# Optimization experiments

Measured on AMD Instinct MI355X. Metric: run time of the kernel, lower is better.

## Reference

```python
import jax, jax.numpy as jnp
import numpy as np
import math

H = 16  # number of heads (init kwarg h)
EPS = 1e-6


def _apply_kernel(x, orf):
    # x: [B, h, L, d_k], orf: [m, d_k]
    m, d_k = orf.shape
    proj = jnp.einsum('bhld,md->bhlm', x, orf) / (d_k ** 0.25)
    norm = jnp.sum(x * x, axis=-1, keepdims=True) / (2.0 * math.sqrt(d_k))
    return (jnp.exp(proj - norm) + EPS) / math.sqrt(m)


def setup_inputs() -> dict:
    key = jax.random.key(0)
    ks = jax.random.split(key, 10)
    B, L, D, m = 4, 4096, 1024, 256
    d_k = D // H
    s = 1.0 / math.sqrt(D)
    return {
        'x': jax.random.normal(ks[0], (B, L, D), jnp.float32),
        'Wq': jax.random.normal(ks[1], (D, D), jnp.float32) * s,
        'bq': jax.random.normal(ks[2], (D,), jnp.float32) * s,
        'Wk': jax.random.normal(ks[3], (D, D), jnp.float32) * s,
        'bk': jax.random.normal(ks[4], (D,), jnp.float32) * s,
        'Wv': jax.random.normal(ks[5], (D, D), jnp.float32) * s,
        'bv': jax.random.normal(ks[6], (D,), jnp.float32) * s,
        'Wo': jax.random.normal(ks[7], (D, D), jnp.float32) * s,
        'bo': jax.random.normal(ks[8], (D,), jnp.float32) * s,
        'orf': jax.random.normal(ks[9], (m, d_k), jnp.float32),
    }


def reference(x, Wq, bq, Wk, bk, Wv, bv, Wo, bo, orf):
    B, L, D = x.shape
    d_k = D // H

    def split(y):  # [B, L, D] -> [B, h, L, d_k]
        return y.reshape(B, L, H, d_k).transpose(0, 2, 1, 3)

    q = split(x @ Wq.T + bq)
    k = split(x @ Wk.T + bk)
    v = split(x @ Wv.T + bv)

    q_phi = _apply_kernel(q, orf)  # [B, h, L, m]
    k_phi = _apply_kernel(k, orf)  # [B, h, L, m]

    # FAVOR+ linear attention: O(L*m*d_k)
    kv = jnp.einsum('bhlm,bhld->bhmd', k_phi, v)      # [B, h, m, d_k]
    ksum = jnp.sum(k_phi, axis=2)                      # [B, h, m]
    num = jnp.einsum('bhlm,bhmd->bhld', q_phi, kv)     # [B, h, L, d_k]
    den = jnp.einsum('bhlm,bhm->bhl', q_phi, ksum)     # [B, h, L]
    out = num / den[..., None]

    out = out.transpose(0, 2, 1, 3).reshape(B, L, D)   # concat heads
    return out @ Wo.T + bo
```

## Files before the change

### kernel.cpp

```cpp
#include <hip/hip_runtime.h>
#include <math.h>

#define HH 16
#define BB 4
#define LL 4096
#define DD 1024
#define DK 64
#define MMF 256
#define EPSF 1e-6f
#define KSCALE (0.35355339059327373f * 1.4426950408889634f)
#define NORMSCALE (0.0625f * 1.4426950408889634f)
#define NSPLIT 8
#define LCH (LL / NSPLIT)

typedef __attribute__((ext_vector_type(8))) short bf16x8;
typedef __attribute__((ext_vector_type(4))) float f32x4;
typedef __attribute__((ext_vector_type(8))) unsigned short u16x8;

__device__ __forceinline__ unsigned short f2bf(float f) {
  union { float f; unsigned u; } v; v.f = f;
  unsigned r = v.u + 0x7FFF + ((v.u >> 16) & 1);
  return (unsigned short)(r >> 16);
}
__device__ __forceinline__ float bf2f(unsigned short h) {
  union { unsigned u; float f; } v; v.u = ((unsigned)h) << 16;
  return v.f;
}
__device__ __forceinline__ f32x4 mfma16(bf16x8 a, bf16x8 b, f32x4 c) {
  return __builtin_amdgcn_mfma_f32_16x16x32_bf16(a, b, c, 0, 0, 0);
}
__device__ __forceinline__ float fexp2(float x) {
  return __builtin_amdgcn_exp2f(x);
}
__device__ __forceinline__ void gload16(const unsigned short* g, unsigned short* l) {
  __builtin_amdgcn_global_load_lds(
      (const __attribute__((address_space(1))) void*)g,
      (__attribute__((address_space(3))) void*)l, 16, 0, 0);
}
#define SWZ(row, col) ((col) ^ (((row) & 7) << 3))

__global__ __launch_bounds__(256) void cvt_bf16(
    const float* __restrict__ src, unsigned short* __restrict__ dst, int n) {
  int i = (blockIdx.x * 256 + threadIdx.x) * 4;
  if (i < n) {
    float4 v = *(const float4*)&src[i];
    ushort4 o;
    o.x = f2bf(v.x); o.y = f2bf(v.y); o.z = f2bf(v.z); o.w = f2bf(v.w);
    *(ushort4*)&dst[i] = o;
  }
}

__global__ __launch_bounds__(256) void cvt_bf16_w(
    const float* __restrict__ W0, const float* __restrict__ W1,
    const float* __restrict__ W2, const float* __restrict__ W3,
    unsigned short* __restrict__ D0, unsigned short* __restrict__ D1,
    unsigned short* __restrict__ D2, unsigned short* __restrict__ D3) {
  const float* s;
  unsigned short* d;
  switch (blockIdx.y) {
    case 0: s = W0; d = D0; break;
    case 1: s = W1; d = D1; break;
    case 2: s = W2; d = D2; break;
    default: s = W3; d = D3; break;
  }
  int i = (blockIdx.x * 256 + threadIdx.x) * 4;
  float4 v = *(const float4*)&s[i];
  ushort4 o;
  o.x = f2bf(v.x); o.y = f2bf(v.y); o.z = f2bf(v.z); o.w = f2bf(v.w);
  *(ushort4*)&d[i] = o;
}

__global__ __launch_bounds__(256) void cvt_orf(
    const float* __restrict__ src, unsigned short* __restrict__ hi, int n) {
  int i = blockIdx.x * 256 + threadIdx.x;
  if (i < n) hi[i] = f2bf(src[i] * KSCALE);
}

template <int MODE>
__global__ __launch_bounds__(256) void gemm_mfma(
    const unsigned short* __restrict__ A, const unsigned short* __restrict__ W,
    const float* __restrict__ bias, float* __restrict__ Cf,
    unsigned short* __restrict__ C1, unsigned short* __restrict__ C2,
    float* __restrict__ Cn, int M, int N, int K) {
  __shared__ __align__(16) char smem[65536];
  unsigned short* S = (unsigned short*)smem;
  const int tid = threadIdx.x, lane = tid & 63;
  const int w = tid >> 6, wr = w >> 1, wc = w & 1;
  const int g = lane >> 4, li = lane & 15;
  const int flat = blockIdx.y * gridDim.x + blockIdx.x;
  const int xcd = flat & 7, loc = flat >> 3;
  const int m0 = ((xcd << 4) + (loc & 15)) * 128;
  const int n0 = (loc >> 4) * 128;

  f32x4 acc[4][4] = {};
  const int srow8 = lane >> 3;
  const int scol  = ((lane & 7) ^ srow8) << 3;
  const unsigned short* Ag = A + (size_t)(m0 + w * 32 + srow8) * K + scol;
  const unsigned short* Wg = W + (size_t)(n0 + w * 32 + srow8) * K + scol;
  const int nt = K >> 6;

#pragma unroll
  for (int j = 0; j < 4; ++j) {
    gload16(Ag + (size_t)j * 8 * K, S + (w * 32 + j * 8) * 64);
    gload16(Wg + (size_t)j * 8 * K, S + 8192 + (w * 32 + j * 8) * 64);
  }

  for (int t = 0; t < nt; ++t) {
    const int co = (t & 1) << 14;
    const int no = co ^ 16384;
    if (t + 1 < nt) {
      const int k1 = (t + 1) << 6;
#pragma unroll
      for (int j = 0; j < 4; ++j) {
        gload16(Ag + (size_t)j * 8 * K + k1, S + no + (w * 32 + j * 8) * 64);
        gload16(Wg + (size_t)j * 8 * K + k1, S + no + 8192 + (w * 32 + j * 8) * 64);
      }
      asm volatile("s_waitcnt vmcnt(8)" ::: "memory");
    } else {
      asm volatile("s_waitcnt vmcnt(0)" ::: "memory");
    }
    __builtin_amdgcn_s_barrier();

    const int sx = (li & 7) << 3;
#pragma unroll
    for (int kk = 0; kk < 2; ++kk) {
      const int c = (kk * 32 + g * 8) ^ sx;
      bf16x8 af[4], bfr[4];
#pragma unroll
      for (int i = 0; i < 4; ++i)
        af[i] = *(const bf16x8*)&S[co + (wr * 64 + i * 16 + li) * 64 + c];
#pragma unroll
      for (int j = 0; j < 4; ++j)
        bfr[j] = *(const bf16x8*)&S[co + 8192 + (wc * 64 + j * 16 + li) * 64 + c];
#pragma unroll
      for (int i = 0; i < 4; ++i)
#pragma unroll
        for (int j = 0; j < 4; ++j)
          acc[i][j] = mfma16(af[i], bfr[j], acc[i][j]);
    }
    asm volatile("s_waitcnt lgkmcnt(0)" ::: "memory");
    __builtin_amdgcn_s_barrier();
  }

  float* ep = (float*)smem + w * (32 * 68);
  const int head = (n0 + wc * 64) >> 6;
  const int rbase = m0 + wr * 64;
  const int b = rbase >> 12;

  if (MODE == 2) {
#pragma unroll
    for (int jh = 0; jh < 2; ++jh) {
#pragma unroll
      for (int i2 = 0; i2 < 2; ++i2) {
        const int i = jh * 2 + i2;
#pragma unroll
        for (int j = 0; j < 4; ++j) {
          const float bz = bias[n0 + wc * 64 + j * 16 + li];
#pragma unroll
          for (int r = 0; r < 4; ++r)
            ep[(i2 * 16 + 4 * g + r) * 68 + j * 16 + li] = acc[i][j][r] + bz;
        }
      }
      const int rrow = lane >> 3, cc = lane & 7;
#pragma unroll
      for (int p = 0; p < 4; ++p) {
        const int row = p * 8 + rrow;
        float v[8];
        *(f32x4*)&v[0] = *(const f32x4*)&ep[row * 68 + cc * 8];
        *(f32x4*)&v[4] = *(const f32x4*)&ep[row * 68 + cc * 8 + 4];
        float np = 0.f;
        u16x8 hv, lv;
#pragma unroll
        for (int e = 0; e < 8; ++e) {
          float vv = v[e];
          np += vv * vv;
          unsigned short h = f2bf(vv);
          hv[e] = h;
          lv[e] = f2bf(vv - bf2f(h));
        }
        const int lg = (rbase + jh * 32 + row) & 4095;
        const size_t rowb = (size_t)(b * 16 + head) * 4096 + lg;
        *(u16x8*)&C1[rowb * 64 + cc * 8] = hv;
        *(u16x8*)&C2[rowb * 64 + cc * 8] = lv;
        np += __shfl_xor(np, 1);
        np += __shfl_xor(np, 2);
        np += __shfl_xor(np, 4);
        if (cc == 0) Cn[rowb] = np * NORMSCALE;
      }
    }
  } else if (MODE == 1) {
#pragma unroll
    for (int jh = 0; jh < 2; ++jh) {
#pragma unroll
      for (int i = 0; i < 4; ++i)
#pragma unroll
        for (int j2 = 0; j2 < 2; ++j2) {
          const int j = jh * 2 + j2;
          const float bz = bias[n0 + wc * 64 + j * 16 + li];
          f32x4 t;
          t[0] = acc[i][j][0] + bz; t[1] = acc[i][j][1] + bz;
          t[2] = acc[i][j][2] + bz; t[3] = acc[i][j][3] + bz;
          *(f32x4*)&ep[(j2 * 16 + li) * 68 + i * 16 + 4 * g] = t;
        }
      const int rd = lane >> 3, cc = lane & 7;
#pragma unroll
      for (int p = 0; p < 4; ++p) {
        const int dl = p * 8 + rd;
        float v[8];
        *(f32x4*)&v[0] = *(const f32x4*)&ep[dl * 68 + cc * 8];
        *(f32x4*)&v[4] = *(const f32x4*)&ep[dl * 68 + cc * 8 + 4];
        u16x8 hv;
#pragma unroll
        for (int e = 0; e < 8; ++e) hv[e] = f2bf(v[e]);
        const int dh = jh * 32 + dl;
        const int lg = rbase & 4095;
        *(u16x8*)&C1[((size_t)(b * 16 + head) * 64 + dh) * 4096 + lg + cc * 8] = hv;
      }
    }
  } else {
#pragma unroll
    for (int jh = 0; jh < 2; ++jh) {
#pragma unroll
      for (int i2 = 0; i2 < 2; ++i2) {
        const int i = jh * 2 + i2;
#pragma unroll
        for (int j = 0; j < 4; ++j) {
          const float bz = bias[n0 + wc * 64 + j * 16 + li];
#pragma unroll
          for (int r = 0; r < 4; ++r)
            ep[(i2 * 16 + 4 * g + r) * 68 + j * 16 + li] = acc[i][j][r] + bz;
        }
      }
      const int rrow = lane >> 4, cc = lane & 15;
#pragma unroll
      for (int p = 0; p < 8; ++p) {
        const int row = p * 4 + rrow;
        f32x4 v = *(const f32x4*)&ep[row * 68 + cc * 4];
        *(f32x4*)&Cf[(size_t)(rbase + jh * 32 + row) * 1024 + n0 + wc * 64 + cc * 4] = v;
      }
    }
  }
}

__global__ __launch_bounds__(256, 2) void kv_mfma(
    const unsigned short* __restrict__ khi, const unsigned short* __restrict__ klo,
    const float* __restrict__ knorms, const unsigned short* __restrict__ vt,
    const unsigned short* __restrict__ orfhi,
    float* __restrict__ pkv, float* __restrict__ pksum) {
  __shared__ __align__(16) unsigned short KsHi[64 * 64], KsLo[64 * 64];
  __shared__ __align__(16) unsigned short VT[64 * 64], KphiT[64 * 64];
  __shared__ float ns[64];
  const int tid = threadIdx.x, lane = tid & 63, w = tid >> 6;
  const int g = lane >> 4, li = lane & 15;
  const int bh = blockIdx.x, sp = blockIdx.y;
  const int srow8 = lane >> 3;
  const int scol  = ((lane & 7) ^ srow8) << 3;
  const int sx = (li & 7) << 3;

  bf16x8 oh[4][2];
#pragma unroll
  for (int p = 0; p < 4; ++p)
#pragma unroll
    for (int kk = 0; kk < 2; ++kk)
      oh[p][kk] = *(const bf16x8*)
          &orfhi[(size_t)(p * 64 + w * 16 + li) * 64 + kk * 32 + g * 8];

  f32x4 kvacc[4][4] = {};
  float ksacc[4][4] = {};

  for (int c = 0; c < LCH / 64; ++c) {
    const int l0 = sp * LCH + c * 64;
    __syncthreads();
    {
      const size_t kb = ((size_t)bh * 4096 + l0 + w * 16 + srow8) * 64 + scol;
      gload16(khi + kb, &KsHi[(w * 16) * 64]);
      gload16(khi + kb + 8 * 64, &KsHi[(w * 16 + 8) * 64]);
      gload16(klo + kb, &KsLo[(w * 16) * 64]);
      gload16(klo + kb + 8 * 64, &KsLo[(w * 16 + 8) * 64]);
      const size_t vb = ((size_t)bh * 64 + w * 16 + srow8) * 4096 + l0 + scol;
      gload16(vt + vb, &VT[(w * 16) * 64]);
      gload16(vt + vb + (size_t)8 * 4096, &VT[(w * 16 + 8) * 64]);
      if (tid < 64) ns[tid] = knorms[(size_t)bh * 4096 + l0 + tid];
    }
    __syncthreads();

#pragma unroll
    for (int p = 0; p < 4; ++p) {
      f32x4 pr[4] = {};
      __builtin_amdgcn_s_setprio(1);
#pragma unroll
      for (int kk = 0; kk < 2; ++kk) {
        const int cx = (kk * 32 + g * 8) ^ sx;
#pragma unroll
        for (int lf = 0; lf < 4; ++lf) {
          const bf16x8 bh2 = *(const bf16x8*)&KsHi[(lf * 16 + li) * 64 + cx];
          const bf16x8 bl2 = *(const bf16x8*)&KsLo[(lf * 16 + li) * 64 + cx];
          pr[lf] = mfma16(oh[p][kk], bh2, pr[lf]);
          pr[lf] = mfma16(oh[p][kk], bl2, pr[lf]);
        }
      }
      __builtin_amdgcn_s_setprio(0);
#pragma unroll
      for (int lf = 0; lf < 4; ++lf) {
        const float nrm = ns[lf * 16 + li];
#pragma unroll
        for (int r = 0; r < 4; ++r) {
          float phi = fexp2(pr[lf][r] - nrm) + EPSF;
          ksacc[p][r] += phi;
          const int row = w * 16 + 4 * g + r;
          KphiT[row * 64 + SWZ(row, lf * 16 + li)] = f2bf(phi);
        }
      }
      __builtin_amdgcn_s_setprio(1);
#pragma unroll
      for (int kk = 0; kk < 2; ++kk) {
        const int cx = (kk * 32 + g * 8) ^ sx;
        const bf16x8 a = *(const bf16x8*)&KphiT[(w * 16 + li) * 64 + cx];
#pragma unroll
        for (int df = 0; df < 4; ++df) {
          const bf16x8 bv = *(const bf16x8*)&VT[(df * 16 + li) * 64 + cx];
          kvacc[p][df] = mfma16(a, bv, kvacc[p][df]);
        }
      }
      __builtin_amdgcn_s_setprio(0);
    }
  }
  float* kvo = pkv + ((size_t)sp * 64 + bh) * (MMF * DK);
#pragma unroll
  for (int p = 0; p < 4; ++p)
#pragma unroll
    for (int df = 0; df < 4; ++df)
#pragma unroll
      for (int r = 0; r < 4; ++r)
        kvo[(p * 64 + w * 16 + 4 * g + r) * DK + df * 16 + li] = kvacc[p][df][r];

  float* kso = pksum + ((size_t)sp * 64 + bh) * MMF;
#pragma unroll
  for (int p = 0; p < 4; ++p)
#pragma unroll
    for (int r = 0; r < 4; ++r) {
      float s = ksacc[p][r];
      s += __shfl_xor(s, 1); s += __shfl_xor(s, 2);
      s += __shfl_xor(s, 4); s += __shfl_xor(s, 8);
      if (li == 0) kso[p * 64 + w * 16 + 4 * g + r] = s;
    }
}

__global__ __launch_bounds__(256) void reduce_parts(
    const float* __restrict__ pkv, unsigned short* __restrict__ kvT,
    const float* __restrict__ pks, float* __restrict__ ksg) {
  const int id = blockIdx.x * 256 + threadIdx.x;
  {
    const int bh = id >> 12, rest = id & 4095;
    const int m0 = (rest >> 6) << 2, d = rest & 63;
    float s0 = 0.f, s1 = 0.f, s2 = 0.f, s3 = 0.f;
#pragma unroll
    for (int sp = 0; sp < NSPLIT; ++sp) {
      const float* p = pkv + (size_t)(sp * 64 + bh) * (MMF * DK) + d;
      s0 += p[(m0 + 0) * DK]; s1 += p[(m0 + 1) * DK];
      s2 += p[(m0 + 2) * DK]; s3 += p[(m0 + 3) * DK];
    }
    ushort4 o;
    o.x = f2bf(s0); o.y = f2bf(s1); o.z = f2bf(s2); o.w = f2bf(s3);
    *(ushort4*)&kvT[((size_t)bh * DK + d) * MMF + m0] = o;
  }
  if (id < 4096) {
    float4 s = {0.f, 0.f, 0.f, 0.f};
#pragma unroll
    for (int sp = 0; sp < NSPLIT; ++sp) {
      float4 v = *(const float4*)&pks[(size_t)sp * 64 * MMF + id * 4];
      s.x += v.x; s.y += v.y; s.z += v.z; s.w += v.w;
    }
    *(float4*)&ksg[id * 4] = s;
  }
}

__global__ __launch_bounds__(512, 4) void qattn_mfma(
    const unsigned short* __restrict__ qhi, const unsigned short* __restrict__ qlo,
    const float* __restrict__ qnorms,
    const unsigned short* __restrict__ orfhi,
    const unsigned short* __restrict__ kvT, const float* __restrict__ ksg,
    unsigned short* __restrict__ attn) {
  __shared__ __align__(16) unsigned short OHi[256 * 64];
  __shared__ __align__(16) unsigned short KvTs[64 * 256];
  __shared__ __align__(16) unsigned short Qphi[8][16 * 64];
  const int tid = threadIdx.x, lane = tid & 63, w = tid >> 6;
  const int g = lane >> 4, li = lane & 15;
  const int bh = blockIdx.x, lb = blockIdx.y;
  const int b = bh >> 4, h = bh & 15;
  const int srow8 = lane >> 3;
  const int scol  = ((lane & 7) ^ srow8) << 3;
  const int sx = (li & 7) << 3;

#pragma unroll
  for (int q = 0; q < 4; ++q) {
    const size_t o = (size_t)(w * 32 + q * 8 + srow8) * 64 + scol;
    gload16(orfhi + o, &OHi[(w * 32 + q * 8) * 64]);
  }
  {
    const int srow2 = lane >> 5;
#pragma unroll
    for (int q = 0; q < 4; ++q) {
      const int d0 = w * 8 + q * 2, dr = d0 + srow2;
      gload16(kvT + ((size_t)bh * DK + dr) * MMF + (((lane & 31) ^ (dr & 7)) << 3),
              &KvTs[d0 * 256]);
    }
  }

  float ksr[4][4];
#pragma unroll
  for (int p = 0; p < 4; ++p)
#pragma unroll
    for (int mf = 0; mf < 4; ++mf)
      ksr[p][mf] = ksg[(size_t)bh * MMF + p * 64 + mf * 16 + li];
  const float4 nr =
      *(const float4*)&qnorms[(size_t)bh * 4096 + lb * 128 + w * 16 + 4 * g];
  bf16x8 qh[2], ql[2];
  {
    const size_t qr = ((size_t)bh * 4096 + lb * 128 + w * 16 + li) * 64 + g * 8;
    qh[0] = *(const bf16x8*)&qhi[qr];
    qh[1] = *(const bf16x8*)&qhi[qr + 32];
    ql[0] = *(const bf16x8*)&qlo[qr];
    ql[1] = *(const bf16x8*)&qlo[qr + 32];
  }
  __syncthreads();

  f32x4 numacc[4] = {};
  float denacc[4] = {};

#pragma unroll
  for (int p = 0; p < 4; ++p) {
    f32x4 pr[4] = {};
    __builtin_amdgcn_s_setprio(1);
#pragma unroll
    for (int kk = 0; kk < 2; ++kk) {
      const int cx = (kk * 32 + g * 8) ^ sx;
#pragma unroll
      for (int mf = 0; mf < 4; ++mf) {
        const int row = p * 64 + mf * 16 + li;
        const bf16x8 bh2 = *(const bf16x8*)&OHi[row * 64 + cx];
        pr[mf] = mfma16(qh[kk], bh2, pr[mf]);
        pr[mf] = mfma16(ql[kk], bh2, pr[mf]);
      }
    }
    __builtin_amdgcn_s_setprio(0);
#pragma unroll
    for (int mf = 0; mf < 4; ++mf) {
      const float ks = ksr[p][mf];
#pragma unroll
      for (int r = 0; r < 4; ++r) {
        float phi = fexp2(pr[mf][r] - nr[r]) + EPSF;
        denacc[r] += phi * ks;
        const int row = 4 * g + r;
        Qphi[w][row * 64 + SWZ(row, mf * 16 + li)] = f2bf(phi);
      }
    }
    __builtin_amdgcn_s_setprio(1);
#pragma unroll
    for (int kk = 0; kk < 2; ++kk) {
      const int cx = (kk * 32 + g * 8) ^ sx;
      const bf16x8 a = *(const bf16x8*)&Qphi[w][li * 64 + cx];
#pragma unroll
      for (int df = 0; df < 4; ++df) {
        const bf16x8 bv = *(const bf16x8*)
            &KvTs[(df * 16 + li) * 256 + (((p * 8 + kk * 4 + g) ^ (li & 7)) << 3)];
        numacc[df] = mfma16(a, bv, numacc[df]);
      }
    }
    __builtin_amdgcn_s_setprio(0);
  }
  float den[4];
#pragma unroll
  for (int r = 0; r < 4; ++r) {
    float s = denacc[r];
    s += __shfl_xor(s, 1); s += __shfl_xor(s, 2);
    s += __shfl_xor(s, 4); s += __shfl_xor(s, 8);
    den[r] = s;
  }
  unsigned short* ab =
      attn + ((size_t)b * 4096 + lb * 128) * 1024 + h * 64;
#pragma unroll
  for (int df = 0; df < 4; ++df)
#pragma unroll
    for (int r = 0; r < 4; ++r)
      ab[(size_t)(w * 16 + 4 * g + r) * 1024 + df * 16 + li] =
          f2bf(numacc[df][r] / den[r]);
}

extern "C" void kernel_launch(void* const* d_in, const int* in_sizes, int n_in,
                              void* d_out, int out_size, void* d_ws, size_t ws_size,
                              hipStream_t stream) {
  (void)in_sizes; (void)n_in; (void)out_size; (void)ws_size;
  const float* x   = (const float*)d_in[0];
  const float* Wq  = (const float*)d_in[1];
  const float* bq  = (const float*)d_in[2];
  const float* Wk  = (const float*)d_in[3];
  const float* bk  = (const float*)d_in[4];
  const float* Wv  = (const float*)d_in[5];
  const float* bv  = (const float*)d_in[6];
  const float* Wo  = (const float*)d_in[7];
  const float* bo  = (const float*)d_in[8];
  const float* orf = (const float*)d_in[9];
  float* out = (float*)d_out;

  const size_t ND = (size_t)BB * LL * DD;
  char* base = (char*)d_ws;
  size_t off = 0;
  auto alloc = [&](size_t bytes) -> char* {
    char* p = base + off;
    off += (bytes + 255) & ~(size_t)255;
    return p;
  };
  unsigned short* wqbf   = (unsigned short*)alloc((size_t)DD * DD * 2);
  unsigned short* wkbf   = (unsigned short*)alloc((size_t)DD * DD * 2);
  unsigned short* wvbf   = (unsigned short*)alloc((size_t)DD * DD * 2);
  unsigned short* wobf   = (unsigned short*)alloc((size_t)DD * DD * 2);
  unsigned short* orfhi  = (unsigned short*)alloc((size_t)MMF * DK * 2);
  unsigned short* xbf    = (unsigned short*)alloc(ND * 2);
  unsigned short* qhi    = (unsigned short*)alloc(ND * 2);
  unsigned short* qlo    = (unsigned short*)alloc(ND * 2);
  unsigned short* khi    = (unsigned short*)alloc(ND * 2);
  unsigned short* klo    = (unsigned short*)alloc(ND * 2);
  unsigned short* vtbuf  = (unsigned short*)alloc(ND * 2);
  float*          qnorms = (float*)alloc((size_t)64 * LL * 4);
  float*          knorms = (float*)alloc((size_t)64 * LL * 4);
  float*          pksum  = (float*)alloc((size_t)NSPLIT * 64 * MMF * 4);
  unsigned short* kvT    = (unsigned short*)alloc((size_t)64 * DK * MMF * 2);
  float*          ksg    = (float*)alloc((size_t)64 * MMF * 4);
  float*          pkv    = (float*)xbf;
  unsigned short* attnbf = khi;

  cvt_bf16<<<16384, 256, 0, stream>>>(x, xbf, (int)ND);
  cvt_bf16_w<<<dim3(1024, 4), 256, 0, stream>>>(Wq, Wk, Wv, Wo,
                                                wqbf, wkbf, wvbf, wobf);
  cvt_orf<<<64, 256, 0, stream>>>(orf, orfhi, MMF * DK);

  dim3 gg(128, 8);
  gemm_mfma<2><<<gg, 256, 0, stream>>>(xbf, wqbf, bq, (float*)0, qhi, qlo,
                                       qnorms, BB * LL, DD, DD);
  gemm_mfma<2><<<gg, 256, 0, stream>>>(xbf, wkbf, bk, (float*)0, khi, klo,
                                       knorms, BB * LL, DD, DD);
  gemm_mfma<1><<<gg, 256, 0, stream>>>(xbf, wvbf, bv, (float*)0, vtbuf,
                                       (unsigned short*)0, (float*)0,
                                       BB * LL, DD, DD);

  kv_mfma<<<dim3(64, NSPLIT), 256, 0, stream>>>(khi, klo, knorms, vtbuf,
                                                orfhi, pkv, pksum);
  reduce_parts<<<1024, 256, 0, stream>>>(pkv, kvT, pksum, ksg);
  qattn_mfma<<<dim3(64, 32), 512, 0, stream>>>(qhi, qlo, qnorms, orfhi,
                                               kvT, ksg, attnbf);

  gemm_mfma<0><<<gg, 256, 0, stream>>>(attnbf, wobf, bo, out, (unsigned short*)0,
                                       (unsigned short*)0, (float*)0,
                                       BB * LL, DD, DD);
}
```

Before: 298.4 us.

## Enlarge GEMM tiles to 256x256 with 8-wave blocks and restructured pipeline

Each of the four projection GEMMs now uses a 256x256 output tile with 512 threads (8 waves, each computing 128x64), a 128KB LDS double buffer, and split k-halves separated by barriers. MFMA sections are wrapped in s_setprio and the epilogues are adjusted for the larger tile, adding barriers between reuses of the LDS staging area. The aim is to raise arithmetic intensity and cut global/LDS traffic per FLOP. In exchange it uses more registers and LDS per block, leaving at most one block per CU and only 256 blocks for 256 CUs, which may cost occupancy and latency hiding.

Measured after the change: 286.5 us. -4.0%, faster.

```diff
diff --git a/kernel.cpp b/kernel.cpp
--- a/kernel.cpp
+++ b/kernel.cpp
@@ -77,85 +77,103 @@
 }
 
 template <int MODE>
-__global__ __launch_bounds__(256) void gemm_mfma(
+__global__ __launch_bounds__(512, 2) void gemm_mfma(
     const unsigned short* __restrict__ A, const unsigned short* __restrict__ W,
     const float* __restrict__ bias, float* __restrict__ Cf,
     unsigned short* __restrict__ C1, unsigned short* __restrict__ C2,
     float* __restrict__ Cn, int M, int N, int K) {
-  __shared__ __align__(16) char smem[65536];
+  __shared__ __align__(16) char smem[131072];
   unsigned short* S = (unsigned short*)smem;
   const int tid = threadIdx.x, lane = tid & 63;
-  const int w = tid >> 6, wr = w >> 1, wc = w & 1;
+  const int w = tid >> 6;
+  const int wm = w >> 2, wn = w & 3;
   const int g = lane >> 4, li = lane & 15;
   const int flat = blockIdx.y * gridDim.x + blockIdx.x;
   const int xcd = flat & 7, loc = flat >> 3;
-  const int m0 = ((xcd << 4) + (loc & 15)) * 128;
-  const int n0 = (loc >> 4) * 128;
-
-  f32x4 acc[4][4] = {};
+  const int m0 = (xcd * 8 + (loc & 7)) * 256;
+  const int n0 = (loc >> 3) * 256;
+
+  f32x4 acc[8][4] = {};
   const int srow8 = lane >> 3;
   const int scol  = ((lane & 7) ^ srow8) << 3;
-  const unsigned short* Ag = A + (size_t)(m0 + w * 32 + srow8) * K + scol;
-  const unsigned short* Wg = W + (size_t)(n0 + w * 32 + srow8) * K + scol;
+  const unsigned short* Ast = A + (size_t)(m0 + w * 32 + srow8) * K + scol;
+  const unsigned short* Wst = W + (size_t)(n0 + w * 32 + srow8) * K + scol;
   const int nt = K >> 6;
-
-#pragma unroll
-  for (int j = 0; j < 4; ++j) {
-    gload16(Ag + (size_t)j * 8 * K, S + (w * 32 + j * 8) * 64);
-    gload16(Wg + (size_t)j * 8 * K, S + 8192 + (w * 32 + j * 8) * 64);
-  }
-
-  for (int t = 0; t < nt; ++t) {
-    const int co = (t & 1) << 14;
-    const int no = co ^ 16384;
-    if (t + 1 < nt) {
-      const int k1 = (t + 1) << 6;
-#pragma unroll
-      for (int j = 0; j < 4; ++j) {
-        gload16(Ag + (size_t)j * 8 * K + k1, S + no + (w * 32 + j * 8) * 64);
-        gload16(Wg + (size_t)j * 8 * K + k1, S + no + 8192 + (w * 32 + j * 8) * 64);
-      }
-      asm volatile("s_waitcnt vmcnt(8)" ::: "memory");
-    } else {
-      asm volatile("s_waitcnt vmcnt(0)" ::: "memory");
-    }
-    __builtin_amdgcn_s_barrier();
-
-    const int sx = (li & 7) << 3;
-#pragma unroll
-    for (int kk = 0; kk < 2; ++kk) {
-      const int c = (kk * 32 + g * 8) ^ sx;
-      bf16x8 af[4], bfr[4];
-#pragma unroll
-      for (int i = 0; i < 4; ++i)
-        af[i] = *(const bf16x8*)&S[co + (wr * 64 + i * 16 + li) * 64 + c];
+  const int sx = (li & 7) << 3;
+
+#pragma unroll
+  for (int gi = 0; gi < 4; ++gi) {
+    gload16(Ast + (size_t)gi * 8 * K, S + (w * 32 + gi * 8) * 64);
+    gload16(Wst + (size_t)gi * 8 * K, S + 16384 + (w * 32 + gi * 8) * 64);
+  }
+  asm volatile("s_waitcnt vmcnt(0)" ::: "memory");
+  __builtin_amdgcn_s_barrier();
+
+  for (int kt = 0; kt < nt; ++kt) {
+    const int co = (kt & 1) << 15;
+    const int no = co ^ 32768;
+    if (kt + 1 < nt) {
+      const size_t k1 = (size_t)(kt + 1) << 6;
+#pragma unroll
+      for (int gi = 0; gi < 4; ++gi) {
+        gload16(Ast + (size_t)gi * 8 * K + k1, S + no + (w * 32 + gi * 8) * 64);
+        gload16(Wst + (size_t)gi * 8 * K + k1,
+                S + no + 16384 + (w * 32 + gi * 8) * 64);
+      }
+    }
+    {
+      const int c = (g * 8) ^ sx;
+      bf16x8 af[8], bfr[4];
+#pragma unroll
+      for (int i = 0; i < 8; ++i)
+        af[i] = *(const bf16x8*)&S[co + (wm * 128 + i * 16 + li) * 64 + c];
 #pragma unroll
       for (int j = 0; j < 4; ++j)
-        bfr[j] = *(const bf16x8*)&S[co + 8192 + (wc * 64 + j * 16 + li) * 64 + c];
-#pragma unroll
-      for (int i = 0; i < 4; ++i)
+        bfr[j] = *(const bf16x8*)&S[co + 16384 + (wn * 64 + j * 16 + li) * 64 + c];
+      __builtin_amdgcn_s_setprio(1);
+#pragma unroll
+      for (int i = 0; i < 8; ++i)
 #pragma unroll
         for (int j = 0; j < 4; ++j)
           acc[i][j] = mfma16(af[i], bfr[j], acc[i][j]);
-    }
-    asm volatile("s_waitcnt lgkmcnt(0)" ::: "memory");
+      __builtin_amdgcn_s_setprio(0);
+    }
     __builtin_amdgcn_s_barrier();
+    {
+      const int c = (32 + g * 8) ^ sx;
+      bf16x8 af[8], bfr[4];
+#pragma unroll
+      for (int i = 0; i < 8; ++i)
+        af[i] = *(const bf16x8*)&S[co + (wm * 128 + i * 16 + li) * 64 + c];
+#pragma unroll
+      for (int j = 0; j < 4; ++j)
+        bfr[j] = *(const bf16x8*)&S[co + 16384 + (wn * 64 + j * 16 + li) * 64 + c];
+      __builtin_amdgcn_s_setprio(1);
+#pragma unroll
+      for (int i = 0; i < 8; ++i)
+#pragma unroll
+        for (int j = 0; j < 4; ++j)
+          acc[i][j] = mfma16(af[i], bfr[j], acc[i][j]);
+      __builtin_amdgcn_s_setprio(0);
+    }
+    if (kt + 1 < nt) asm volatile("s_waitcnt vmcnt(0)" ::: "memory");
+    __builtin_amdgcn_s_barrier();
   }
 
   float* ep = (float*)smem + w * (32 * 68);
-  const int head = (n0 + wc * 64) >> 6;
-  const int rbase = m0 + wr * 64;
+  const int head = (n0 + wn * 64) >> 6;
+  const int rbase = m0 + wm * 128;
   const int b = rbase >> 12;
 
   if (MODE == 2) {
 #pragma unroll
-    for (int jh = 0; jh < 2; ++jh) {
+    for (int jh = 0; jh < 4; ++jh) {
 #pragma unroll
       for (int i2 = 0; i2 < 2; ++i2) {
         const int i = jh * 2 + i2;
 #pragma unroll
         for (int j = 0; j < 4; ++j) {
-          const float bz = bias[n0 + wc * 64 + j * 16 + li];
+          const float bz = bias[n0 + wn * 64 + j * 16 + li];
 #pragma unroll
           for (int r = 0; r < 4; ++r)
             ep[(i2 * 16 + 4 * g + r) * 68 + j * 16 + li] = acc[i][j][r] + bz;
@@ -187,45 +205,52 @@
         np += __shfl_xor(np, 4);
         if (cc == 0) Cn[rowb] = np * NORMSCALE;
       }
+      __builtin_amdgcn_s_barrier();
     }
   } else if (MODE == 1) {
 #pragma unroll
     for (int jh = 0; jh < 2; ++jh) {
 #pragma unroll
-      for (int i = 0; i < 4; ++i)
-#pragma unroll
-        for (int j2 = 0; j2 < 2; ++j2) {
-          const int j = jh * 2 + j2;
-          const float bz = bias[n0 + wc * 64 + j * 16 + li];
-          f32x4 t;
-          t[0] = acc[i][j][0] + bz; t[1] = acc[i][j][1] + bz;
-          t[2] = acc[i][j][2] + bz; t[3] = acc[i][j][3] + bz;
-          *(f32x4*)&ep[(j2 * 16 + li) * 68 + i * 16 + 4 * g] = t;
-        }
-      const int rd = lane >> 3, cc = lane & 7;
-#pragma unroll
-      for (int p = 0; p < 4; ++p) {
-        const int dl = p * 8 + rd;
-        float v[8];
-        *(f32x4*)&v[0] = *(const f32x4*)&ep[dl * 68 + cc * 8];
-        *(f32x4*)&v[4] = *(const f32x4*)&ep[dl * 68 + cc * 8 + 4];
-        u16x8 hv;
-#pragma unroll
-        for (int e = 0; e < 8; ++e) hv[e] = f2bf(v[e]);
-        const int dh = jh * 32 + dl;
-        const int lg = rbase & 4095;
-        *(u16x8*)&C1[((size_t)(b * 16 + head) * 64 + dh) * 4096 + lg + cc * 8] = hv;
+      for (int lh = 0; lh < 2; ++lh) {
+#pragma unroll
+        for (int i2 = 0; i2 < 4; ++i2) {
+          const int i = lh * 4 + i2;
+#pragma unroll
+          for (int j2 = 0; j2 < 2; ++j2) {
+            const int j = jh * 2 + j2;
+            const float bz = bias[n0 + wn * 64 + j * 16 + li];
+            f32x4 t;
+            t[0] = acc[i][j][0] + bz; t[1] = acc[i][j][1] + bz;
+            t[2] = acc[i][j][2] + bz; t[3] = acc[i][j][3] + bz;
+            *(f32x4*)&ep[(j2 * 16 + li) * 68 + i2 * 16 + 4 * g] = t;
+          }
+        }
+        const int rd = lane >> 3, cc = lane & 7;
+#pragma unroll
+        for (int p = 0; p < 4; ++p) {
+          const int dl = p * 8 + rd;
+          float v[8];
+          *(f32x4*)&v[0] = *(const f32x4*)&ep[dl * 68 + cc * 8];
+          *(f32x4*)&v[4] = *(const f32x4*)&ep[dl * 68 + cc * 8 + 4];
+          u16x8 hv;
+#pragma unroll
+          for (int e = 0; e < 8; ++e) hv[e] = f2bf(v[e]);
+          const int dh = jh * 32 + dl;
+          const int lg = (rbase + lh * 64) & 4095;
+          *(u16x8*)&C1[((size_t)(b * 16 + head) * 64 + dh) * 4096 + lg + cc * 8] = hv;
+        }
+        __builtin_amdgcn_s_barrier();
       }
     }
   } else {
 #pragma unroll
-    for (int jh = 0; jh < 2; ++jh) {
+    for (int jh = 0; jh < 4; ++jh) {
 #pragma unroll
       for (int i2 = 0; i2 < 2; ++i2) {
         const int i = jh * 2 + i2;
 #pragma unroll
         for (int j = 0; j < 4; ++j) {
-          const float bz = bias[n0 + wc * 64 + j * 16 + li];
+          const float bz = bias[n0 + wn * 64 + j * 16 + li];
 #pragma unroll
           for (int r = 0; r < 4; ++r)
             ep[(i2 * 16 + 4 * g + r) * 68 + j * 16 + li] = acc[i][j][r] + bz;
@@ -236,8 +261,9 @@
       for (int p = 0; p < 8; ++p) {
         const int row = p * 4 + rrow;
         f32x4 v = *(const f32x4*)&ep[row * 68 + cc * 4];
-        *(f32x4*)&Cf[(size_t)(rbase + jh * 32 + row) * 1024 + n0 + wc * 64 + cc * 4] = v;
-      }
+        *(f32x4*)&Cf[(size_t)(rbase + jh * 32 + row) * 1024 + n0 + wn * 64 + cc * 4] = v;
+      }
+      __builtin_amdgcn_s_barrier();
     }
   }
 }
@@ -535,12 +561,12 @@
                                                 wqbf, wkbf, wvbf, wobf);
   cvt_orf<<<64, 256, 0, stream>>>(orf, orfhi, MMF * DK);
 
-  dim3 gg(128, 8);
-  gemm_mfma<2><<<gg, 256, 0, stream>>>(xbf, wqbf, bq, (float*)0, qhi, qlo,
+  dim3 gg(64, 4);
+  gemm_mfma<2><<<gg, 512, 0, stream>>>(xbf, wqbf, bq, (float*)0, qhi, qlo,
                                        qnorms, BB * LL, DD, DD);
-  gemm_mfma<2><<<gg, 256, 0, stream>>>(xbf, wkbf, bk, (float*)0, khi, klo,
+  gemm_mfma<2><<<gg, 512, 0, stream>>>(xbf, wkbf, bk, (float*)0, khi, klo,
                                        knorms, BB * LL, DD, DD);
-  gemm_mfma<1><<<gg, 256, 0, stream>>>(xbf, wvbf, bv, (float*)0, vtbuf,
+  gemm_mfma<1><<<gg, 512, 0, stream>>>(xbf, wvbf, bv, (float*)0, vtbuf,
                                        (unsigned short*)0, (float*)0,
                                        BB * LL, DD, DD);
 
@@ -550,7 +576,7 @@
   qattn_mfma<<<dim3(64, 32), 512, 0, stream>>>(qhi, qlo, qnorms, orfhi,
                                                kvT, ksg, attnbf);
 
-  gemm_mfma<0><<<gg, 256, 0, stream>>>(attnbf, wobf, bo, out, (unsigned short*)0,
+  gemm_mfma<0><<<gg, 512, 0, stream>>>(attnbf, wobf, bo, out, (unsigned short*)0,
                                        (unsigned short*)0, (float*)0,
                                        BB * LL, DD, DD);
 }
```

## Use 256x128 GEMM tiles with 512 threads and a triple-buffered LDS pipeline

Applied to the files above, without the earlier changes.

Reworks the bf16 MFMA GEMM used for the Q/K/V/O projections. Each block now computes a 256x128 output tile with 8 waves instead of 128x128 with 4 waves, which halves the grid and cuts the W traffic per output. The double-buffered K loop becomes a three-stage LDS pipeline that prefetches two tiles ahead. The MFMA sections are wrapped in s_setprio. The cost is 144KB of LDS per block, which likely limits each CU to one block and lowers occupancy.

Measured after the change: 303.9 us. Within noise of the previous version (+1.8%).

```diff
diff --git a/kernel.cpp b/kernel.cpp
--- a/kernel.cpp
+++ b/kernel.cpp
@@ -77,74 +77,82 @@
 }
 
 template <int MODE>
-__global__ __launch_bounds__(256) void gemm_mfma(
+__global__ __launch_bounds__(512, 2) void gemm_mfma(
     const unsigned short* __restrict__ A, const unsigned short* __restrict__ W,
     const float* __restrict__ bias, float* __restrict__ Cf,
     unsigned short* __restrict__ C1, unsigned short* __restrict__ C2,
     float* __restrict__ Cn, int M, int N, int K) {
-  __shared__ __align__(16) char smem[65536];
+  __shared__ __align__(16) char smem[147456];
   unsigned short* S = (unsigned short*)smem;
   const int tid = threadIdx.x, lane = tid & 63;
-  const int w = tid >> 6, wr = w >> 1, wc = w & 1;
+  const int w = tid >> 6;
+  const int wm = w >> 1, wn = w & 1;
   const int g = lane >> 4, li = lane & 15;
   const int flat = blockIdx.y * gridDim.x + blockIdx.x;
   const int xcd = flat & 7, loc = flat >> 3;
-  const int m0 = ((xcd << 4) + (loc & 15)) * 128;
-  const int n0 = (loc >> 4) * 128;
+  const int m0 = (xcd * 8 + (loc & 7)) * 256;
+  const int n0 = (loc >> 3) * 128;
 
   f32x4 acc[4][4] = {};
   const int srow8 = lane >> 3;
   const int scol  = ((lane & 7) ^ srow8) << 3;
-  const unsigned short* Ag = A + (size_t)(m0 + w * 32 + srow8) * K + scol;
-  const unsigned short* Wg = W + (size_t)(n0 + w * 32 + srow8) * K + scol;
+  const unsigned short* Ast = A + (size_t)(m0 + w * 32 + srow8) * K + scol;
+  const unsigned short* Wst = W + (size_t)(n0 + w * 16 + srow8) * K + scol;
   const int nt = K >> 6;
-
-#pragma unroll
-  for (int j = 0; j < 4; ++j) {
-    gload16(Ag + (size_t)j * 8 * K, S + (w * 32 + j * 8) * 64);
-    gload16(Wg + (size_t)j * 8 * K, S + 8192 + (w * 32 + j * 8) * 64);
-  }
-
-  for (int t = 0; t < nt; ++t) {
-    const int co = (t & 1) << 14;
-    const int no = co ^ 16384;
-    if (t + 1 < nt) {
-      const int k1 = (t + 1) << 6;
-#pragma unroll
-      for (int j = 0; j < 4; ++j) {
-        gload16(Ag + (size_t)j * 8 * K + k1, S + no + (w * 32 + j * 8) * 64);
-        gload16(Wg + (size_t)j * 8 * K + k1, S + no + 8192 + (w * 32 + j * 8) * 64);
-      }
-      asm volatile("s_waitcnt vmcnt(8)" ::: "memory");
-    } else {
-      asm volatile("s_waitcnt vmcnt(0)" ::: "memory");
-    }
-    __builtin_amdgcn_s_barrier();
-
-    const int sx = (li & 7) << 3;
+  const int sx = (li & 7) << 3;
+
+#define STAGE(buf, kt_)                                                        \
+  {                                                                            \
+    const size_t ko_ = (size_t)(kt_) << 6;                                     \
+    _Pragma("unroll")                                                          \
+    for (int gi = 0; gi < 4; ++gi)                                             \
+      gload16(Ast + (size_t)gi * 8 * K + ko_,                                  \
+              S + (buf) + (w * 32 + gi * 8) * 64);                             \
+    _Pragma("unroll")                                                          \
+    for (int gi = 0; gi < 2; ++gi)                                             \
+      gload16(Wst + (size_t)gi * 8 * K + ko_,                                  \
+              S + (buf) + 16384 + (w * 16 + gi * 8) * 64);                     \
+  }
+
+  STAGE(0, 0)
+  STAGE(24576, 1)
+  asm volatile("s_waitcnt vmcnt(6)" ::: "memory");
+  __builtin_amdgcn_s_barrier();
+
+  int b0 = 0, b1 = 24576, b2 = 49152;
+  for (int kt = 0; kt < nt; ++kt) {
+    if (kt + 2 < nt) STAGE(b2, kt + 2)
 #pragma unroll
     for (int kk = 0; kk < 2; ++kk) {
       const int c = (kk * 32 + g * 8) ^ sx;
       bf16x8 af[4], bfr[4];
 #pragma unroll
       for (int i = 0; i < 4; ++i)
-        af[i] = *(const bf16x8*)&S[co + (wr * 64 + i * 16 + li) * 64 + c];
+        af[i] = *(const bf16x8*)&S[b0 + (wm * 64 + i * 16 + li) * 64 + c];
 #pragma unroll
       for (int j = 0; j < 4; ++j)
-        bfr[j] = *(const bf16x8*)&S[co + 8192 + (wc * 64 + j * 16 + li) * 64 + c];
+        bfr[j] = *(const bf16x8*)&S[b0 + 16384 + (wn * 64 + j * 16 + li) * 64 + c];
+      __builtin_amdgcn_s_setprio(1);
 #pragma unroll
       for (int i = 0; i < 4; ++i)
 #pragma unroll
         for (int j = 0; j < 4; ++j)
           acc[i][j] = mfma16(af[i], bfr[j], acc[i][j]);
+      __builtin_amdgcn_s_setprio(0);
     }
     asm volatile("s_waitcnt lgkmcnt(0)" ::: "memory");
+    if (kt + 2 < nt) {
+      asm volatile("s_waitcnt vmcnt(6)" ::: "memory");
+    } else if (kt + 1 < nt) {
+      asm volatile("s_waitcnt vmcnt(0)" ::: "memory");
+    }
     __builtin_amdgcn_s_barrier();
+    const int tmp = b0; b0 = b1; b1 = b2; b2 = tmp;
   }
 
   float* ep = (float*)smem + w * (32 * 68);
-  const int head = (n0 + wc * 64) >> 6;
-  const int rbase = m0 + wr * 64;
+  const int head = (n0 + wn * 64) >> 6;
+  const int rbase = m0 + wm * 64;
   const int b = rbase >> 12;
 
   if (MODE == 2) {
@@ -155,7 +163,7 @@
         const int i = jh * 2 + i2;
 #pragma unroll
         for (int j = 0; j < 4; ++j) {
-          const float bz = bias[n0 + wc * 64 + j * 16 + li];
+          const float bz = bias[n0 + wn * 64 + j * 16 + li];
 #pragma unroll
           for (int r = 0; r < 4; ++r)
             ep[(i2 * 16 + 4 * g + r) * 68 + j * 16 + li] = acc[i][j][r] + bz;
@@ -196,7 +204,7 @@
 #pragma unroll
         for (int j2 = 0; j2 < 2; ++j2) {
           const int j = jh * 2 + j2;
-          const float bz = bias[n0 + wc * 64 + j * 16 + li];
+          const float bz = bias[n0 + wn * 64 + j * 16 + li];
           f32x4 t;
           t[0] = acc[i][j][0] + bz; t[1] = acc[i][j][1] + bz;
           t[2] = acc[i][j][2] + bz; t[3] = acc[i][j][3] + bz;
@@ -225,7 +233,7 @@
         const int i = jh * 2 + i2;
 #pragma unroll
         for (int j = 0; j < 4; ++j) {
-          const float bz = bias[n0 + wc * 64 + j * 16 + li];
+          const float bz = bias[n0 + wn * 64 + j * 16 + li];
 #pragma unroll
           for (int r = 0; r < 4; ++r)
             ep[(i2 * 16 + 4 * g + r) * 68 + j * 16 + li] = acc[i][j][r] + bz;
@@ -236,10 +244,11 @@
       for (int p = 0; p < 8; ++p) {
         const int row = p * 4 + rrow;
         f32x4 v = *(const f32x4*)&ep[row * 68 + cc * 4];
-        *(f32x4*)&Cf[(size_t)(rbase + jh * 32 + row) * 1024 + n0 + wc * 64 + cc * 4] = v;
-      }
-    }
-  }
+        *(f32x4*)&Cf[(size_t)(rbase + jh * 32 + row) * 1024 + n0 + wn * 64 + cc * 4] = v;
+      }
+    }
+  }
+#undef STAGE
 }
 
 __global__ __launch_bounds__(256, 2) void kv_mfma(
@@ -535,12 +544,12 @@
                                                 wqbf, wkbf, wvbf, wobf);
   cvt_orf<<<64, 256, 0, stream>>>(orf, orfhi, MMF * DK);
 
-  dim3 gg(128, 8);
-  gemm_mfma<2><<<gg, 256, 0, stream>>>(xbf, wqbf, bq, (float*)0, qhi, qlo,
+  dim3 gg(64, 8);
+  gemm_mfma<2><<<gg, 512, 0, stream>>>(xbf, wqbf, bq, (float*)0, qhi, qlo,
                                        qnorms, BB * LL, DD, DD);
-  gemm_mfma<2><<<gg, 256, 0, stream>>>(xbf, wkbf, bk, (float*)0, khi, klo,
+  gemm_mfma<2><<<gg, 512, 0, stream>>>(xbf, wkbf, bk, (float*)0, khi, klo,
                                        knorms, BB * LL, DD, DD);
-  gemm_mfma<1><<<gg, 256, 0, stream>>>(xbf, wvbf, bv, (float*)0, vtbuf,
+  gemm_mfma<1><<<gg, 512, 0, stream>>>(xbf, wvbf, bv, (float*)0, vtbuf,
                                        (unsigned short*)0, (float*)0,
                                        BB * LL, DD, DD);
 
@@ -550,7 +559,7 @@
   qattn_mfma<<<dim3(64, 32), 512, 0, stream>>>(qhi, qlo, qnorms, orfhi,
                                                kvT, ksg, attnbf);
 
-  gemm_mfma<0><<<gg, 256, 0, stream>>>(attnbf, wobf, bo, out, (unsigned short*)0,
+  gemm_mfma<0><<<gg, 512, 0, stream>>>(attnbf, wobf, bo, out, (unsigned short*)0,
                                        (unsigned short*)0, (float*)0,
                                        BB * LL, DD, DD);
 }
```
